# Kernel optimization log

Measured on AMD Instinct MI355X. Metric: run time of the kernel, lower is better.

The kernel has to match this reference:

```python
import jax, jax.numpy as jnp
import numpy as np

K = 1024          # number of breakpoints in the LUT
N_ROWS = 4096
N_COLS = 16384


def setup_inputs() -> dict:
    key = jax.random.key(0)
    k1, k2, k3, k4 = jax.random.split(key, 4)
    # Breakpoints must be sorted for the LUT semantics (sum(d > x) == searchsorted).
    x = jnp.sort(jax.random.normal(k1, (K,), dtype=jnp.float32) * 3.0)
    a = jax.random.normal(k2, (K + 1,), dtype=jnp.float32)  # per-segment slope
    b = jax.random.normal(k3, (K + 1,), dtype=jnp.float32)  # per-segment intercept
    data = jax.random.normal(k4, (N_ROWS, N_COLS), dtype=jnp.float32)
    return {"data": data, "x": x, "a": a, "b": b}


def reference(data, x, a, b):
    # Original: index = sum(d > x_i) over breakpoints. With x sorted ascending this
    # equals the number of breakpoints strictly less than d, i.e.
    # searchsorted(x, d, side='left'). This avoids the [N, K] compare matrix.
    d = data.reshape(-1)
    index = jnp.searchsorted(x, d, side="left")  # int32 in [0, K]
    out = a[index] * d + b[index]                 # gather + FMA, one pass
    return out.reshape(data.shape)
```

## Files before the change

kernel.cpp:

```cpp
#include <hip/hip_runtime.h>


#define LUT_K 1024
#define NB    8192
#define WS_NEEDED (NB * 2 + 8)

__device__ __forceinline__ int bucket_of(float v, float x0, float invw) {
    int t = (int)__fmul_rn(__fsub_rn(v, x0), invw);
    t = t < 0 ? 0 : t;
    return t > (NB - 1) ? (NB - 1) : t;
}

__global__ __launch_bounds__(256) void build_kernel(const float* __restrict__ x, void* ws) {
    __shared__ float xs[LUT_K];
    unsigned short* bs = (unsigned short*)ws;
    float* params = (float*)((char*)ws + NB * 2);
    for (int i = threadIdx.x; i < LUT_K; i += blockDim.x) xs[i] = x[i];
    __syncthreads();
    const float x0 = xs[0];
    const float invw = (float)NB / (xs[LUT_K - 1] - x0);
    if (blockIdx.x == 0 && threadIdx.x == 0) { params[0] = x0; params[1] = invw; }
    int j = blockIdx.x * blockDim.x + threadIdx.x;
    if (j < NB) {
        int lo = 0, hi = LUT_K;
        while (lo < hi) {
            int mid = (lo + hi) >> 1;
            if (bucket_of(xs[mid], x0, invw) < j) lo = mid + 1; else hi = mid;
        }
        bs[j] = (unsigned short)lo;
    }
}

__global__ __launch_bounds__(256) void lut_main(
    const float* __restrict__ data, const float* __restrict__ x,
    const float* __restrict__ a, const float* __restrict__ b,
    const void* __restrict__ ws, float* __restrict__ out, int n4, int use_ws)
{
    __shared__ float xs[LUT_K + 1];
    __shared__ float aa[LUT_K + 1];
    __shared__ float bb[LUT_K + 1];
    __shared__ __align__(16) unsigned short bs[NB];

    for (int i = threadIdx.x; i < LUT_K; i += blockDim.x) xs[i] = x[i];
    for (int i = threadIdx.x; i < LUT_K + 1; i += blockDim.x) { aa[i] = a[i]; bb[i] = b[i]; }
    if (threadIdx.x == 0) xs[LUT_K] = __builtin_inff();

    float x0, invw;
    if (use_ws) {
        const float* params = (const float*)((const char*)ws + NB * 2);
        x0 = params[0]; invw = params[1];
        const uint2* gbs = (const uint2*)ws;
        for (int i = threadIdx.x; i < NB / 4; i += blockDim.x)
            ((uint2*)bs)[i] = gbs[i];
        __syncthreads();
    } else {
        __syncthreads();
        x0 = xs[0];
        invw = (float)NB / (xs[LUT_K - 1] - x0);
        for (int j = threadIdx.x; j < NB; j += blockDim.x) {
            int lo = 0, hi = LUT_K;
            while (lo < hi) {
                int mid = (lo + hi) >> 1;
                if (bucket_of(xs[mid], x0, invw) < j) lo = mid + 1; else hi = mid;
            }
            bs[j] = (unsigned short)lo;
        }
        __syncthreads();
    }

    const float4* __restrict__ in4 = (const float4*)data;
    float4* __restrict__ out4 = (float4*)out;

    auto eval = [&](float v) -> float {
        int j = bucket_of(v, x0, invw);
        int idx = bs[j];
        while (xs[idx] < v) idx++;
        return fmaf(aa[idx], v, bb[idx]);
    };

    const int stride = gridDim.x * blockDim.x;
    for (int i = blockIdx.x * blockDim.x + threadIdx.x; i < n4; i += stride) {
        float4 d = in4[i];
        float4 r;
        r.x = eval(d.x);
        r.y = eval(d.y);
        r.z = eval(d.z);
        r.w = eval(d.w);
        out4[i] = r;
    }
}

extern "C" void kernel_launch(void* const* d_in, const int* in_sizes, int n_in,
                              void* d_out, int out_size, void* d_ws, size_t ws_size,
                              hipStream_t stream) {
    const float* data = (const float*)d_in[0];
    const float* x    = (const float*)d_in[1];
    const float* a    = (const float*)d_in[2];
    const float* b    = (const float*)d_in[3];
    float* out = (float*)d_out;

    int n  = in_sizes[0];
    int n4 = n >> 2;

    int use_ws = (ws_size >= (size_t)WS_NEEDED) ? 1 : 0;
    if (use_ws)
        build_kernel<<<(NB + 255) / 256, 256, 0, stream>>>(x, d_ws);

    lut_main<<<1280, 256, 0, stream>>>(data, x, a, b, d_ws, out, n4, use_ws);
}
```

Measured before the change: 440.8 us.

## Pack bucket count into LUT records, interleave slope/intercept, prefetch next input

Each bucket record now stores the start index plus a saturated count of the breakpoints inside the bucket, so the lookup does a fixed-count branchless compare loop instead of a data-dependent while loop. Slopes and intercepts are interleaved into one float2 shared array so a single LDS read fetches both. The main grid-stride loop software-prefetches the next float4 of input to overlap the global load with the evaluation. In exchange the build does two binary searches per bucket, and lookups can still diverge across lanes whose buckets hold different counts.

Measured after the change: 450.6 us. 1.02x slower.

```diff
diff --git a/kernel.cpp b/kernel.cpp
--- a/kernel.cpp
+++ b/kernel.cpp
@@ -3,6 +3,7 @@
 
 #define LUT_K 1024
 #define NB    8192
+#define CNT_SAT 31
 #define WS_NEEDED (NB * 2 + 8)
 
 __device__ __forceinline__ int bucket_of(float v, float x0, float invw) {
@@ -11,9 +12,19 @@
     return t > (NB - 1) ? (NB - 1) : t;
 }
 
+__device__ __forceinline__ int lower_bound_bucket(const float* xs, float x0,
+                                                  float invw, int target) {
+    int lo = 0, hi = LUT_K;
+    while (lo < hi) {
+        int mid = (lo + hi) >> 1;
+        if (bucket_of(xs[mid], x0, invw) < target) lo = mid + 1; else hi = mid;
+    }
+    return lo;
+}
+
 __global__ __launch_bounds__(256) void build_kernel(const float* __restrict__ x, void* ws) {
     __shared__ float xs[LUT_K];
-    unsigned short* bs = (unsigned short*)ws;
+    unsigned short* recs = (unsigned short*)ws;
     float* params = (float*)((char*)ws + NB * 2);
     for (int i = threadIdx.x; i < LUT_K; i += blockDim.x) xs[i] = x[i];
     __syncthreads();
@@ -22,12 +33,10 @@
     if (blockIdx.x == 0 && threadIdx.x == 0) { params[0] = x0; params[1] = invw; }
     int j = blockIdx.x * blockDim.x + threadIdx.x;
     if (j < NB) {
-        int lo = 0, hi = LUT_K;
-        while (lo < hi) {
-            int mid = (lo + hi) >> 1;
-            if (bucket_of(xs[mid], x0, invw) < j) lo = mid + 1; else hi = mid;
-        }
-        bs[j] = (unsigned short)lo;
+        int lo  = lower_bound_bucket(xs, x0, invw, j);
+        int lo2 = lower_bound_bucket(xs, x0, invw, j + 1);
+        int cnt = lo2 - lo; if (cnt > CNT_SAT) cnt = CNT_SAT;
+        recs[j] = (unsigned short)(lo | (cnt << 11));
     }
 }
 
@@ -37,33 +46,31 @@
     const void* __restrict__ ws, float* __restrict__ out, int n4, int use_ws)
 {
     __shared__ float xs[LUT_K + 1];
-    __shared__ float aa[LUT_K + 1];
-    __shared__ float bb[LUT_K + 1];
-    __shared__ __align__(16) unsigned short bs[NB];
+    __shared__ __align__(16) float2 ab[LUT_K + 1];
+    __shared__ __align__(16) unsigned short recs[NB];
 
     for (int i = threadIdx.x; i < LUT_K; i += blockDim.x) xs[i] = x[i];
-    for (int i = threadIdx.x; i < LUT_K + 1; i += blockDim.x) { aa[i] = a[i]; bb[i] = b[i]; }
+    for (int i = threadIdx.x; i < LUT_K + 1; i += blockDim.x)
+        ab[i] = make_float2(a[i], b[i]);
     if (threadIdx.x == 0) xs[LUT_K] = __builtin_inff();
 
     float x0, invw;
     if (use_ws) {
         const float* params = (const float*)((const char*)ws + NB * 2);
         x0 = params[0]; invw = params[1];
-        const uint2* gbs = (const uint2*)ws;
-        for (int i = threadIdx.x; i < NB / 4; i += blockDim.x)
-            ((uint2*)bs)[i] = gbs[i];
+        const uint2* gr = (const uint2*)ws;
+        uint2* lr = (uint2*)recs;
+        for (int i = threadIdx.x; i < NB / 4; i += blockDim.x) lr[i] = gr[i];
         __syncthreads();
     } else {
         __syncthreads();
         x0 = xs[0];
         invw = (float)NB / (xs[LUT_K - 1] - x0);
         for (int j = threadIdx.x; j < NB; j += blockDim.x) {
-            int lo = 0, hi = LUT_K;
-            while (lo < hi) {
-                int mid = (lo + hi) >> 1;
-                if (bucket_of(xs[mid], x0, invw) < j) lo = mid + 1; else hi = mid;
-            }
-            bs[j] = (unsigned short)lo;
+            int lo  = lower_bound_bucket(xs, x0, invw, j);
+            int lo2 = lower_bound_bucket(xs, x0, invw, j + 1);
+            int cnt = lo2 - lo; if (cnt > CNT_SAT) cnt = CNT_SAT;
+            recs[j] = (unsigned short)(lo | (cnt << 11));
         }
         __syncthreads();
     }
@@ -73,20 +80,39 @@
 
     auto eval = [&](float v) -> float {
         int j = bucket_of(v, x0, invw);
-        int idx = bs[j];
-        while (xs[idx] < v) idx++;
-        return fmaf(aa[idx], v, bb[idx]);
+        unsigned r = recs[j];
+        int idx = (int)(r & 0x7FFu);
+        int cnt = (int)(r >> 11);
+        if (cnt) {
+            int base = idx;
+            if (cnt == CNT_SAT) {
+                while (xs[idx] < v) idx++;
+            } else {
+                for (int t = 0; t < cnt; ++t)
+                    idx += (xs[base + t] < v) ? 1 : 0;
+            }
+        }
+        float2 p = ab[idx];
+        return fmaf(p.x, v, p.y);
     };
 
     const int stride = gridDim.x * blockDim.x;
-    for (int i = blockIdx.x * blockDim.x + threadIdx.x; i < n4; i += stride) {
-        float4 d = in4[i];
+    int i = blockIdx.x * blockDim.x + threadIdx.x;
+    bool have = i < n4;
+    float4 d = make_float4(0.f, 0.f, 0.f, 0.f);
+    if (have) d = in4[i];
+    while (have) {
+        int ni = i + stride;
+        bool have_n = ni < n4;
+        float4 dn = make_float4(0.f, 0.f, 0.f, 0.f);
+        if (have_n) dn = in4[ni];
         float4 r;
         r.x = eval(d.x);
         r.y = eval(d.y);
         r.z = eval(d.z);
         r.w = eval(d.w);
         out4[i] = r;
+        i = ni; d = dn; have = have_n;
     }
 }
 
```
